# Kernel tuning notes

Hardware: AMD Instinct MI355X
Metric: run time of the kernel (lower is better)

Reference implementation:

```python
import jax, jax.numpy as jnp
import numpy as np

NUM_KEYS = 64

def setup_inputs() -> dict:
    key = jax.random.key(0)
    k1, k2 = jax.random.split(key)
    inputs = jax.random.randint(k1, (8, 4096, 1024), 0, NUM_KEYS, dtype=jnp.int32)
    # learned per-key bias (build() creates shape (num_keys,) for key_shape=[1])
    b = jax.random.normal(k2, (NUM_KEYS,), dtype=jnp.float32)
    # keys are sorted unique scalars (0..63), stored as float like the TF cast
    keys = jnp.arange(NUM_KEYS, dtype=jnp.float32)
    return {"inputs": inputs, "b": b, "keys": keys}


def reference(inputs, b, keys):
    # Original math: out = sum_k (inputs == keys[k]) * b[k], elementwise over inputs.
    # With unique sorted keys this is a gather: find the matching key index per
    # element and pick b there; elements matching no key contribute 0.
    # This avoids the O(num_keys * numel) broadcast blow-up of the TF graph.
    xf = inputs.astype(jnp.float32)
    K = keys.shape[0]
    idx = jnp.clip(jnp.searchsorted(keys, xf), 0, K - 1)  # [8,4096,1024]
    out = jnp.where(keys[idx] == xf, b[idx], jnp.float32(0.0))
    return out
```

## Files before the change

### kernel.cpp

```cpp
#include <hip/hip_runtime.h>

#define NKEYS 64

__global__ __launch_bounds__(256) void sel_xform_kernel(
    const int4* __restrict__ in,
    const float* __restrict__ b,
    const float* __restrict__ keys,
    float4* __restrict__ out,
    int nvec, int ntail, const int* __restrict__ in_tail, float* __restrict__ out_tail)
{
    __shared__ float t[NKEYS];
    const int tid = threadIdx.x;
    if (tid < NKEYS) t[tid] = 0.0f;
    __syncthreads();
    if (tid < NKEYS) {
        const float kv = keys[tid];
        const int iv = (int)kv;
        if ((float)iv == kv && iv >= 0 && iv < NKEYS) {
            t[iv] = b[tid];
        }
    }
    __syncthreads();

    int i = blockIdx.x * blockDim.x + tid;
    const int stride = gridDim.x * blockDim.x;
    for (; i < nvec; i += stride) {
        const int4 v = in[i];
        float4 o;
        o.x = ((unsigned)v.x < NKEYS) ? t[v.x] : 0.0f;
        o.y = ((unsigned)v.y < NKEYS) ? t[v.y] : 0.0f;
        o.z = ((unsigned)v.z < NKEYS) ? t[v.z] : 0.0f;
        o.w = ((unsigned)v.w < NKEYS) ? t[v.w] : 0.0f;
        out[i] = o;
    }

    if (blockIdx.x == 0 && tid < ntail) {
        const int v = in_tail[tid];
        out_tail[tid] = ((unsigned)v < NKEYS) ? t[v] : 0.0f;
    }
}

extern "C" void kernel_launch(void* const* d_in, const int* in_sizes, int n_in,
                              void* d_out, int out_size, void* d_ws, size_t ws_size,
                              hipStream_t stream) {
    const int*   x    = (const int*)d_in[0];
    const float* b    = (const float*)d_in[1];
    const float* keys = (const float*)d_in[2];
    float* out = (float*)d_out;

    const int n    = in_sizes[0];
    const int nvec = n >> 2;
    const int ntail = n & 3;

    const int block = 256;
    int grid = (nvec + block - 1) / block;
    if (grid < 1) grid = 1;

    sel_xform_kernel<<<grid, block, 0, stream>>>(
        (const int4*)x, b, keys, (float4*)out,
        nvec, ntail, x + (nvec << 2), out + (nvec << 2));
}
```

Before: 225.2 us.

## Use wave-level bpermute lookup, nontemporal stores, prefetch loop, capped grid

Each lane now holds one table entry in a register, and the per-element gather uses ds_bpermute across the 64-lane wavefront instead of indexed shared-memory reads. A grid-stride loop with a capped grid software-prefetches the next int4 input before the current one is processed. Output is written with nontemporal stores to avoid polluting the cache. The intent is to cut LDS bank conflicts and keep more loads in flight on a bandwidth-bound streaming kernel. The cost is fewer blocks and added register and loop complexity.

Result: slower. 233.1 us (+3.5%).

```diff
diff --git a/kernel.cpp b/kernel.cpp
--- a/kernel.cpp
+++ b/kernel.cpp
@@ -1,12 +1,14 @@
 #include <hip/hip_runtime.h>
 
 #define NKEYS 64
+
+typedef float vfloat4 __attribute__((ext_vector_type(4)));
 
 __global__ __launch_bounds__(256) void sel_xform_kernel(
     const int4* __restrict__ in,
     const float* __restrict__ b,
     const float* __restrict__ keys,
-    float4* __restrict__ out,
+    float* __restrict__ out,
     int nvec, int ntail, const int* __restrict__ in_tail, float* __restrict__ out_tail)
 {
     __shared__ float t[NKEYS];
@@ -22,16 +24,40 @@
     }
     __syncthreads();
 
+    const int tv_i = __float_as_int(t[tid & 63]);
+
     int i = blockIdx.x * blockDim.x + tid;
     const int stride = gridDim.x * blockDim.x;
-    for (; i < nvec; i += stride) {
-        const int4 v = in[i];
-        float4 o;
-        o.x = ((unsigned)v.x < NKEYS) ? t[v.x] : 0.0f;
-        o.y = ((unsigned)v.y < NKEYS) ? t[v.y] : 0.0f;
-        o.z = ((unsigned)v.z < NKEYS) ? t[v.z] : 0.0f;
-        o.w = ((unsigned)v.w < NKEYS) ? t[v.w] : 0.0f;
-        out[i] = o;
+
+    if (i < nvec) {
+        int4 v = in[i];
+        int inext = i + stride;
+        while (inext < nvec) {
+            const int4 vn = in[inext];
+            vfloat4 o;
+            o.x = __int_as_float(__builtin_amdgcn_ds_bpermute(v.x << 2, tv_i));
+            o.y = __int_as_float(__builtin_amdgcn_ds_bpermute(v.y << 2, tv_i));
+            o.z = __int_as_float(__builtin_amdgcn_ds_bpermute(v.z << 2, tv_i));
+            o.w = __int_as_float(__builtin_amdgcn_ds_bpermute(v.w << 2, tv_i));
+            if ((unsigned)v.x >= NKEYS) o.x = 0.0f;
+            if ((unsigned)v.y >= NKEYS) o.y = 0.0f;
+            if ((unsigned)v.z >= NKEYS) o.z = 0.0f;
+            if ((unsigned)v.w >= NKEYS) o.w = 0.0f;
+            __builtin_nontemporal_store(o, (vfloat4*)&out[i << 2]);
+            v = vn;
+            i = inext;
+            inext += stride;
+        }
+        vfloat4 o;
+        o.x = __int_as_float(__builtin_amdgcn_ds_bpermute(v.x << 2, tv_i));
+        o.y = __int_as_float(__builtin_amdgcn_ds_bpermute(v.y << 2, tv_i));
+        o.z = __int_as_float(__builtin_amdgcn_ds_bpermute(v.z << 2, tv_i));
+        o.w = __int_as_float(__builtin_amdgcn_ds_bpermute(v.w << 2, tv_i));
+        if ((unsigned)v.x >= NKEYS) o.x = 0.0f;
+        if ((unsigned)v.y >= NKEYS) o.y = 0.0f;
+        if ((unsigned)v.z >= NKEYS) o.z = 0.0f;
+        if ((unsigned)v.w >= NKEYS) o.w = 0.0f;
+        __builtin_nontemporal_store(o, (vfloat4*)&out[i << 2]);
     }
 
     if (blockIdx.x == 0 && tid < ntail) {
@@ -48,15 +74,16 @@
     const float* keys = (const float*)d_in[2];
     float* out = (float*)d_out;
 
-    const int n    = in_sizes[0];
-    const int nvec = n >> 2;
+    const int n     = in_sizes[0];
+    const int nvec  = n >> 2;
     const int ntail = n & 3;
 
     const int block = 256;
     int grid = (nvec + block - 1) / block;
+    if (grid > 8192) grid = 8192;
     if (grid < 1) grid = 1;
 
     sel_xform_kernel<<<grid, block, 0, stream>>>(
-        (const int4*)x, b, keys, (float4*)out,
+        (const int4*)x, b, keys, out,
         nvec, ntail, x + (nvec << 2), out + (nvec << 2));
 }
```
